# Performance work log

Measured on AMD Instinct MI355X. Metric: run time of the kernel, lower is better.

The kernel has to match this reference:

```python
import jax, jax.numpy as jnp
import numpy as np

DILATION = 6
KS = 3
N = KS * KS  # 9 kernel sample points
PAD = 1      # zero padding inside DeformConv2d
EPS = 1e-5


def conv2d(x, w, b=None, padding=0):
    out = jax.lax.conv_general_dilated(
        x, w, window_strides=(1, 1),
        padding=[(padding, padding), (padding, padding)],
        dimension_numbers=('NCHW', 'OIHW', 'NCHW'))
    if b is not None:
        out = out + b[None, :, None, None]
    return out


def batchnorm_train(x, gamma, beta):
    # training-mode BN (module default): batch statistics over (N,H,W)
    mean = x.mean(axis=(0, 2, 3), keepdims=True)
    var = x.var(axis=(0, 2, 3), keepdims=True)
    return gamma[None, :, None, None] * (x - mean) * jax.lax.rsqrt(var + EPS) + beta[None, :, None, None]


def deform_conv(x, p_w, p_b, m_w, m_b, d_w, d_b, w):
    b, c, h, wd = x.shape
    offset = conv2d(x, p_w, p_b, padding=1)                 # (b, 2N, h, w)
    m = jax.nn.sigmoid(conv2d(x, m_w, m_b, padding=1))      # (b, N, h, w) modulation
    s = 2.0 * jax.nn.sigmoid(conv2d(x, d_w, d_b, padding=1))  # (b,1,h,w) adaptive dilation scale (=1 at logit 0)
    xp = jnp.pad(x, ((0, 0), (0, 0), (PAD, PAD), (PAD, PAD)))
    Hp, Wp = h + 2 * PAD, wd + 2 * PAD
    # kernel grid p_n, row-major (kh, kw) to match conv weight layout
    rng = jnp.arange(-(KS - 1) // 2, (KS - 1) // 2 + 1, dtype=x.dtype)
    pn_x, pn_y = jnp.meshgrid(rng, rng, indexing='ij')
    pn_x, pn_y = pn_x.reshape(-1), pn_y.reshape(-1)          # (N,)
    # base sampling positions (offset by PAD into padded map)
    p0_x = jnp.arange(1, h + 1, dtype=x.dtype)[:, None, None]    # (h,1,1)
    p0_y = jnp.arange(1, wd + 1, dtype=x.dtype)[None, :, None]   # (1,w,1)
    off = offset.transpose(0, 2, 3, 1)   # (b,h,w,2N)
    s_ = s.transpose(0, 2, 3, 1)         # (b,h,w,1)
    px = p0_x + DILATION * s_ * pn_x + off[..., :N]   # (b,h,w,N)
    py = p0_y + DILATION * s_ * pn_y + off[..., N:]
    fx, fy = jnp.floor(px), jnp.floor(py)
    qx_lt = jnp.clip(fx, 0, Hp - 1).astype(jnp.int32)
    qy_lt = jnp.clip(fy, 0, Wp - 1).astype(jnp.int32)
    qx_rb = jnp.clip(fx + 1, 0, Hp - 1).astype(jnp.int32)
    qy_rb = jnp.clip(fy + 1, 0, Wp - 1).astype(jnp.int32)
    pxc = jnp.clip(px, 0, Hp - 1)
    pyc = jnp.clip(py, 0, Wp - 1)
    g_lt = (1 + (qx_lt - pxc)) * (1 + (qy_lt - pyc))
    g_rb = (1 - (qx_rb - pxc)) * (1 - (qy_rb - pyc))
    g_lb = (1 + (qx_lt - pxc)) * (1 - (qy_rb - pyc))
    g_rt = (1 - (qx_rb - pxc)) * (1 + (qy_lt - pyc))

    def gather(qx, qy):
        idx = (qx * Wp + qy).reshape(b, 1, -1)                    # (b,1,h*w*N)
        xf = xp.reshape(b, c, Hp * Wp)
        out = jnp.take_along_axis(xf, jnp.broadcast_to(idx, (b, c, idx.shape[-1])), axis=2)
        return out.reshape(b, c, h, wd, N)

    x_off = (g_lt[:, None] * gather(qx_lt, qy_lt)
             + g_rb[:, None] * gather(qx_rb, qy_rb)
             + g_lb[:, None] * gather(qx_lt, qy_rb)
             + g_rt[:, None] * gather(qx_rb, qy_lt))
    x_off = x_off * m.transpose(0, 2, 3, 1)[:, None]              # modulation
    # final 3x3 conv over gathered samples == contraction over (c, N)
    return jnp.einsum('bchwn,ocn->bohw', x_off, w.reshape(w.shape[0], c, N))


def setup_inputs() -> dict:
    key = jax.random.key(0)
    ks = jax.random.split(key, 12)
    cin, c1, c2 = 512, 256, 64
    b, h, w = 2, 96, 96
    def rn(k, shape, scale):
        return jax.random.normal(k, shape, dtype=jnp.float32) * scale
    return {
        'x': rn(ks[0], (b, cin, h, w), 1.0),
        'bn1_g': jnp.ones((cin,), jnp.float32),
        'bn1_b': jnp.zeros((cin,), jnp.float32),
        'conv1_w': rn(ks[1], (c1, cin, 1, 1), (1.0 / cin) ** 0.5),
        'conv1_b': jnp.zeros((c1,), jnp.float32),
        'bn2_g': jnp.ones((c1,), jnp.float32),
        'bn2_b': jnp.zeros((c1,), jnp.float32),
        'p_w': rn(ks[2], (2 * N, c1, 3, 3), 0.01),
        'p_b': jnp.zeros((2 * N,), jnp.float32),
        'm_w': rn(ks[3], (N, c1, 3, 3), 0.01),
        'm_b': jnp.zeros((N,), jnp.float32),
        'd_w': rn(ks[4], (1, c1, 3, 3), 0.01),
        'd_b': jnp.zeros((1,), jnp.float32),
        'dconv_w': rn(ks[5], (c2, c1, 3, 3), (1.0 / (c1 * 9)) ** 0.5),
    }


def reference(x, bn1_g, bn1_b, conv1_w, conv1_b, bn2_g, bn2_b,
              p_w, p_b, m_w, m_b, d_w, d_b, dconv_w):
    f = jax.nn.relu(batchnorm_train(x, bn1_g, bn1_b))
    f = conv2d(f, conv1_w, conv1_b)
    f = batchnorm_train(f, bn2_g, bn2_b)
    return deform_conv(f, p_w, p_b, m_w, m_b, d_w, d_b, dconv_w)
```

## Files before the change

kernel.cpp:

```cpp
#include <hip/hip_runtime.h>
#include <hip/hip_bf16.h>
#include <math.h>

#define BATCH 2
#define CIN 512
#define C1 256
#define C2 64
#define HH 96
#define WW 96
#define HWSZ 9216
#define NPIX 18432
#define HP 98
#define WP 98
#define PLSTRIDE 516096

typedef __attribute__((ext_vector_type(8))) short bf16x8;
typedef __attribute__((ext_vector_type(4))) short bf16x4;
typedef __attribute__((ext_vector_type(4))) float f32x4;
typedef __attribute__((ext_vector_type(4))) unsigned int u32x4;
typedef __attribute__((ext_vector_type(2))) unsigned int u32x2;
typedef unsigned short u16;
typedef unsigned int u32;

__device__ __forceinline__ float bfu2f(u16 u) {
  u32 v = ((u32)u) << 16; return __builtin_bit_cast(float, v);
}
__device__ __forceinline__ u16 f2bfu(float f) {
  return __builtin_bit_cast(u16, __float2bfloat16(f));
}
__device__ __forceinline__ float rd_any(const void* p, size_t i, int fl) {
  return fl ? bfu2f(((const u16*)p)[i]) : ((const float*)p)[i];
}
__device__ __forceinline__ int get_fl(const u32* g1raw) {
  return g1raw[0] != 0x3F800000u;
}
__device__ __forceinline__ bf16x8 lds_frag(const u16* p) {
  bf16x4 lo = *(const bf16x4*)p;
  bf16x4 hi = *(const bf16x4*)(p + 4);
  bf16x8 r;
  r[0] = lo[0]; r[1] = lo[1]; r[2] = lo[2]; r[3] = lo[3];
  r[4] = hi[0]; r[5] = hi[1]; r[6] = hi[2]; r[7] = hi[3];
  return r;
}
__device__ __forceinline__ void split4(const f32x4& v, u32x2& ph, u32x2& pl) {
  u16 h0 = f2bfu(v[0]), h1 = f2bfu(v[1]), h2 = f2bfu(v[2]), h3 = f2bfu(v[3]);
  u16 l0 = f2bfu(v[0] - bfu2f(h0)), l1 = f2bfu(v[1] - bfu2f(h1));
  u16 l2 = f2bfu(v[2] - bfu2f(h2)), l3 = f2bfu(v[3] - bfu2f(h3));
  ph = (u32x2){(u32)h0 | ((u32)h1 << 16), (u32)h2 | ((u32)h3 << 16)};
  pl = (u32x2){(u32)l0 | ((u32)l1 << 16), (u32)l2 | ((u32)l3 << 16)};
}

__global__ __launch_bounds__(256) void prep_kernel(
    const void* cw, const void* pw, const void* mw, const void* dw, const void* dcw,
    const void* cb, const void* g1, const void* b1, const void* g2, const void* b2,
    const void* pb, const void* mb, const void* db,
    u16* __restrict__ W1b, u16* __restrict__ W1l,
    u16* __restrict__ Wofa, u16* __restrict__ Wofal,
    u16* __restrict__ Wab, u16* __restrict__ Wabl,
    float* __restrict__ canon, float* __restrict__ statz, float* __restrict__ xpf) {
  int e = blockIdx.x * 256 + threadIdx.x;
  if (e >= 555036) return;
  int fl = get_fl((const u32*)g1);
  if (e < 131072) {
    float v = rd_any(cw, e, fl);
    u16 h = f2bfu(v);
    W1b[e] = h; W1l[e] = f2bfu(v - bfu2f(h));
  } else if (e < 204800) {
    int i = e - 131072;
    int tap = i >> 13; int r = i & 8191; int m = r >> 8; int c = r & 255;
    float v = 0.f;
    if (m < 18)       v = rd_any(pw, (size_t)(m * 256 + c) * 9 + tap, fl);
    else if (m < 27)  v = rd_any(mw, (size_t)((m - 18) * 256 + c) * 9 + tap, fl);
    else if (m == 27) v = rd_any(dw, (size_t)c * 9 + tap, fl);
    u16 h = f2bfu(v);
    Wofa[i] = h; Wofal[i] = f2bfu(v - bfu2f(h));
  } else if (e < 352256) {
    int i = e - 204800;
    int n = i >> 14; int r = i & 16383; int o = r >> 8; int c = r & 255;
    float v = rd_any(dcw, (size_t)(o * 256 + c) * 9 + n, fl);
    u16 h = f2bfu(v);
    Wab[i] = h; Wabl[i] = f2bfu(v - bfu2f(h));
  } else if (e < 354076) {
    int i = e - 352256;
    const void* src; int off;
    if      (i < 256)  { src = cb; off = i; }
    else if (i < 768)  { src = g1; off = i - 256; }
    else if (i < 1280) { src = b1; off = i - 768; }
    else if (i < 1536) { src = g2; off = i - 1280; }
    else if (i < 1792) { src = b2; off = i - 1536; }
    else if (i < 1810) { src = pb; off = i - 1792; }
    else if (i < 1819) { src = mb; off = i - 1810; }
    else               { src = db; off = i - 1819; }
    canon[i] = rd_any(src, off, fl);
  } else if (e < 356380) {
    statz[e - 354076] = 0.f;
  } else {
    int k = e - 356380;
    int ch = k & 255; int pxi = k >> 8;
    int bb = pxi / 388; int r = pxi % 388;
    int h, w;
    if (r < 98)      { h = 0;  w = r; }
    else if (r < 196){ h = 97; w = r - 98; }
    else if (r < 292){ h = r - 196 + 1; w = 0; }
    else             { h = r - 292 + 1; w = 97; }
    xpf[(((size_t)(bb * HP) + h) * WP + w) * C1 + ch] = 0.f;
  }
}

__global__ __launch_bounds__(256) void bn_stats_kernel(
    const void* __restrict__ x, const float* __restrict__ gamma,
    const float* __restrict__ beta, float* __restrict__ scale,
    float* __restrict__ shift, float* __restrict__ sums, float* __restrict__ sumsq,
    int* __restrict__ cnt, const u32* __restrict__ g1raw, int force, int C) {
  int c = blockIdx.x, part = blockIdx.y, tid = threadIdx.x;
  int fl = force ? 1 : get_fl(g1raw);
  int b = part >> 1, half = part & 1;
  size_t base = ((size_t)(b * C + c)) * HWSZ + half * (HWSZ / 2);
  float s = 0.f, q = 0.f;
  if (fl) {
    const u16* p = (const u16*)x + base;
    for (int i = tid; i < 576; i += 256) {
      u32x4 U = *(const u32x4*)(p + i * 8);
      #pragma unroll
      for (int k = 0; k < 4; ++k) {
        float v0 = bfu2f((u16)(U[k] & 0xffff));
        float v1 = bfu2f((u16)(U[k] >> 16));
        s += v0 + v1; q = fmaf(v0, v0, fmaf(v1, v1, q));
      }
    }
  } else {
    const float* p = (const float*)x + base;
    for (int i = tid; i < 1152; i += 256) {
      f32x4 v = *(const f32x4*)(p + i * 4);
      #pragma unroll
      for (int k = 0; k < 4; ++k) { s += v[k]; q = fmaf(v[k], v[k], q); }
    }
  }
  __shared__ float sh[512];
  sh[tid] = s; sh[tid + 256] = q;
  __syncthreads();
  for (int off = 128; off > 0; off >>= 1) {
    if (tid < off) { sh[tid] += sh[tid + off]; sh[tid + 256] += sh[tid + 256 + off]; }
    __syncthreads();
  }
  if (tid == 0) {
    atomicAdd(&sums[c], sh[0]);
    atomicAdd(&sumsq[c], sh[256]);
    __threadfence();
    int old = atomicAdd(&cnt[c], 1);
    if (old == 3) {
      float S = atomicAdd(&sums[c], 0.f);
      float Q = atomicAdd(&sumsq[c], 0.f);
      float mean = S * (1.f / (float)NPIX);
      float var  = fmaxf(Q * (1.f / (float)NPIX) - mean * mean, 0.f);
      float sc = gamma[c] * rsqrtf(var + 1e-5f);
      scale[c] = sc;
      shift[c] = beta[c] - mean * sc;
    }
  }
}

__global__ __launch_bounds__(256) void conv1x1_kernel(
    const void* __restrict__ x, const u16* __restrict__ W1b, const u16* __restrict__ W1l,
    const float* __restrict__ cb, const float* __restrict__ scale,
    const float* __restrict__ shift, const u32* __restrict__ g1raw,
    u16* __restrict__ f1) {
  __shared__ u16 Bh[2][64][68];
  __shared__ u16 Bl[2][64][68];
  int tid = threadIdx.x;
  int fl = get_fl(g1raw);
  int bxr = blockIdx.x;
  int bx = (bxr & 7) * 36 + (bxr >> 3);
  int p0 = bx * 64;
  int co0 = blockIdx.y * 128;
  int b = p0 / HWSZ;
  int hw0 = p0 % HWSZ;
  int lane = tid & 63, wv = tid >> 6, quad = lane >> 4, mr = lane & 15;
  int m0 = co0 + wv * 32;
  f32x4 acc[2][4];
  #pragma unroll
  for (int i = 0; i < 2; ++i)
    #pragma unroll
    for (int j = 0; j < 4; ++j) acc[i][j] = (f32x4){0.f, 0.f, 0.f, 0.f};

  int spx = tid & 63, cg = tid >> 6;
  int gpx = hw0 + spx;

  float pva[8], pvb[8];
  auto ISSUE = [&](int c0) {
    #pragma unroll
    for (int j = 0; j < 8; ++j) {
      int ci = c0 + cg * 16 + j * 2;
      if (fl) {
        const u16* xb = (const u16*)x;
        pva[j] = bfu2f(xb[((size_t)(b * CIN + ci)) * HWSZ + gpx]);
        pvb[j] = bfu2f(xb[((size_t)(b * CIN + ci + 1)) * HWSZ + gpx]);
      } else {
        const float* xf = (const float*)x;
        pva[j] = xf[((size_t)(b * CIN + ci)) * HWSZ + gpx];
        pvb[j] = xf[((size_t)(b * CIN + ci + 1)) * HWSZ + gpx];
      }
    }
  };
  auto COMBINE = [&](int buf, int c0) {
    #pragma unroll
    for (int j = 0; j < 8; ++j) {
      int ci = c0 + cg * 16 + j * 2;
      float v0 = fmaxf(fmaf(pva[j], scale[ci], shift[ci]), 0.f);
      float v1 = fmaxf(fmaf(pvb[j], scale[ci + 1], shift[ci + 1]), 0.f);
      u16 h0 = f2bfu(v0), h1 = f2bfu(v1);
      u16 l0 = f2bfu(v0 - bfu2f(h0)), l1 = f2bfu(v1 - bfu2f(h1));
      *(u32*)&Bh[buf][spx][cg * 16 + j * 2] = (u32)h0 | ((u32)h1 << 16);
      *(u32*)&Bl[buf][spx][cg * 16 + j * 2] = (u32)l0 | ((u32)l1 << 16);
    }
  };

  ISSUE(0);
  COMBINE(0, 0);
  for (int c8 = 0; c8 < 8; ++c8) {
    __syncthreads();
    if (c8 < 7) ISSUE((c8 + 1) * 64);
    int bsel = c8 & 1;
    int c0 = c8 * 64;
    #pragma unroll
    for (int kk2 = 0; kk2 < 2; ++kk2) {
      int kk = kk2 * 32;
      #pragma unroll
      for (int mf = 0; mf < 2; ++mf) {
        size_t wix = (size_t)(m0 + mf * 16 + mr) * CIN + c0 + kk + quad * 8;
        bf16x8 ah = *(const bf16x8*)(W1b + wix);
        bf16x8 al = *(const bf16x8*)(W1l + wix);
        #pragma unroll
        for (int nt = 0; nt < 4; ++nt) {
          bf16x8 bl = lds_frag(&Bl[bsel][nt * 16 + mr][kk + quad * 8]);
          bf16x8 bh = lds_frag(&Bh[bsel][nt * 16 + mr][kk + quad * 8]);
          acc[mf][nt] = __builtin_amdgcn_mfma_f32_16x16x32_bf16(ah, bl, acc[mf][nt], 0, 0, 0);
          acc[mf][nt] = __builtin_amdgcn_mfma_f32_16x16x32_bf16(al, bh, acc[mf][nt], 0, 0, 0);
          acc[mf][nt] = __builtin_amdgcn_mfma_f32_16x16x32_bf16(ah, bh, acc[mf][nt], 0, 0, 0);
        }
      }
    }
    if (c8 < 7) COMBINE(bsel ^ 1, (c8 + 1) * 64);
  }
  #pragma unroll
  for (int mf = 0; mf < 2; ++mf) {
    #pragma unroll
    for (int nt = 0; nt < 4; ++nt) {
      #pragma unroll
      for (int r = 0; r < 4; ++r) {
        int co = m0 + mf * 16 + quad * 4 + r;
        f1[((size_t)(b * C1 + co)) * HWSZ + hw0 + nt * 16 + mr] = f2bfu(acc[mf][nt][r] + cb[co]);
      }
    }
  }
}

__global__ __launch_bounds__(256) void bn2pad_kernel(
    const u16* __restrict__ f1, const float* __restrict__ scale,
    const float* __restrict__ shift, float* __restrict__ xpf) {
  int bid = blockIdx.x;
  int ht = bid % 144; int ct = (bid / 144) & 3; int b = bid / 576;
  int hw0 = ht * 64, c0 = ct * 64;
  __shared__ float t[64][65];
  int tid = threadIdx.x;
  #pragma unroll
  for (int it = 0; it < 16; ++it) {
    int e = it * 256 + tid;
    int p = e & 63, ci = e >> 6;
    float v = bfu2f(f1[((size_t)(b * C1 + c0 + ci)) * HWSZ + hw0 + p]);
    t[ci][p] = fmaf(v, scale[c0 + ci], shift[c0 + ci]);
  }
  __syncthreads();
  #pragma unroll
  for (int it = 0; it < 16; ++it) {
    int e = it * 256 + tid;
    int ci = e & 63, p = e >> 6;
    int hw = hw0 + p; int h = hw / WW; int w = hw % WW;
    xpf[(((size_t)(b * HP) + h + 1) * WP + w + 1) * C1 + c0 + ci] = t[ci][p];
  }
}

__global__ __launch_bounds__(256) void offconv_kernel(
    const float* __restrict__ xpf, const u16* __restrict__ Wofa, const u16* __restrict__ Wofal,
    const float* __restrict__ pbc, const float* __restrict__ mbc,
    const float* __restrict__ dbc, float* __restrict__ opart3) {
  __shared__ u16 Vh[2][32][68];
  __shared__ u16 Vl[2][32][68];
  int tid = threadIdx.x;
  int bxr = blockIdx.x;
  int bx = (bxr & 7) * 72 + (bxr >> 3);
  int tg = blockIdx.y;
  int p0 = bx * 32;
  int b = p0 / HWSZ;
  int hw = p0 % HWSZ; int h0 = hw / WW; int w0 = hw % WW;
  int lane = tid & 63, wv = tid >> 6, quad = lane >> 4, mr = lane & 15;
  int m0 = (wv & 1) * 16;
  int ntile = wv >> 1;
  int srow = tid >> 4;
  int scol = (tid & 15) * 4;
  f32x4 acc = (f32x4){0.f, 0.f, 0.f, 0.f};

  f32x4 pvA[2], pvB[2];
  auto ISSUE = [&](f32x4 (&pv)[2], int it) {
    int tap = tg * 3 + (it >> 2);
    int th = tap / 3, tw = tap % 3;
    int c0 = (it & 3) * 64;
    const float* base = xpf + ((size_t)(b * HP + h0 + th) * WP + (w0 + tw)) * C1;
    #pragma unroll
    for (int pass = 0; pass < 2; ++pass) {
      int px = pass * 16 + srow;
      pv[pass] = *(const f32x4*)(base + (size_t)px * C1 + c0 + scol);
    }
  };
  auto COMBINE = [&](f32x4 (&pv)[2], int buf) {
    #pragma unroll
    for (int pass = 0; pass < 2; ++pass) {
      int px = pass * 16 + srow;
      u32x2 ph, pl;
      split4(pv[pass], ph, pl);
      *(u32x2*)&Vh[buf][px][scol] = ph;
      *(u32x2*)&Vl[buf][px][scol] = pl;
    }
  };
  auto MFMA_STEP = [&](int bsel, int it) {
    int tap = tg * 3 + (it >> 2);
    int c0 = (it & 3) * 64;
    #pragma unroll
    for (int kk2 = 0; kk2 < 2; ++kk2) {
      int kof = kk2 * 32 + quad * 8;
      size_t wix = (size_t)(tap * 32 + m0 + mr) * C1 + c0 + kof;
      bf16x8 ah = *(const bf16x8*)(Wofa + wix);
      bf16x8 al = *(const bf16x8*)(Wofal + wix);
      bf16x8 bl = lds_frag(&Vl[bsel][ntile * 16 + mr][kof]);
      bf16x8 bh = lds_frag(&Vh[bsel][ntile * 16 + mr][kof]);
      acc = __builtin_amdgcn_mfma_f32_16x16x32_bf16(ah, bl, acc, 0, 0, 0);
      acc = __builtin_amdgcn_mfma_f32_16x16x32_bf16(al, bh, acc, 0, 0, 0);
      acc = __builtin_amdgcn_mfma_f32_16x16x32_bf16(ah, bh, acc, 0, 0, 0);
    }
  };

  ISSUE(pvA, 0);
  ISSUE(pvB, 1);
  COMBINE(pvA, 0);
  for (int it = 0; it < 12; it += 2) {
    __syncthreads();
    if (it + 2 < 12) ISSUE(pvA, it + 2);
    MFMA_STEP(0, it);
    COMBINE(pvB, 1);
    __syncthreads();
    if (it + 3 < 12) ISSUE(pvB, it + 3);
    MFMA_STEP(1, it + 1);
    if (it + 2 < 12) COMBINE(pvA, 0);
  }
  float* plane = opart3 + (size_t)tg * PLSTRIDE;
  int px = ntile * 16 + mr;
  #pragma unroll
  for (int r = 0; r < 4; ++r) {
    int m = m0 + quad * 4 + r;
    if (m < 28) {
      float v = acc[r];
      if (tg == 0) v += (m < 18) ? pbc[m] : ((m < 27) ? mbc[m - 18] : dbc[0]);
      plane[(size_t)m * NPIX + p0 + px] = v;
    }
  }
}

__global__ __launch_bounds__(256) void deform_kernel(
    const float* __restrict__ xpf, const u16* __restrict__ Wab, const u16* __restrict__ Wabl,
    const float* __restrict__ opart3, float* __restrict__ planes3) {
  __shared__ u16   Vh[2][32][68];
  __shared__ u16   Vl[2][32][68];
  __shared__ int   smi[3][4][32];
  __shared__ float smw[3][4][32];
  int tid = threadIdx.x;
  int bxr = blockIdx.x;
  int bx = (bxr & 7) * 72 + (bxr >> 3);
  int g = blockIdx.y;
  int p0 = bx * 32;
  int b = p0 / HWSZ;
  int hw0 = p0 % HWSZ;

  if (tid < 96) {
    int nn = tid >> 5;
    int p = tid & 31;
    int n = g * 3 + nn;
    int bp = p0 + p;
    int hw = hw0 + p; int h = hw / WW; int w = hw % WW;
    const float* P0 = opart3;
    const float* P1 = opart3 + PLSTRIDE;
    const float* P2 = opart3 + 2 * PLSTRIDE;
    size_t iox = (size_t)n * NPIX + bp;
    size_t ioy = (size_t)(9 + n) * NPIX + bp;
    size_t iml = (size_t)(18 + n) * NPIX + bp;
    size_t isl = (size_t)27 * NPIX + bp;
    float offx = P0[iox] + P1[iox] + P2[iox];
    float offy = P0[ioy] + P1[ioy] + P2[ioy];
    float mlog = P0[iml] + P1[iml] + P2[iml];
    float slog = P0[isl] + P1[isl] + P2[isl];
    float mm = 1.f / (1.f + expf(-mlog));
    float s  = 2.f / (1.f + expf(-slog));
    float pnx = (float)(n / 3 - 1), pny = (float)(n % 3 - 1);
    float px = (float)(h + 1) + 6.f * s * pnx + offx;
    float py = (float)(w + 1) + 6.f * s * pny + offy;
    float fx = floorf(px), fy = floorf(py);
    float qxlt = fminf(fmaxf(fx, 0.f), 97.f);
    float qylt = fminf(fmaxf(fy, 0.f), 97.f);
    float qxrb = fminf(fmaxf(fx + 1.f, 0.f), 97.f);
    float qyrb = fminf(fmaxf(fy + 1.f, 0.f), 97.f);
    float pxc = fminf(fmaxf(px, 0.f), 97.f);
    float pyc = fminf(fmaxf(py, 0.f), 97.f);
    float glt = (1.f + (qxlt - pxc)) * (1.f + (qylt - pyc));
    float grb = (1.f - (qxrb - pxc)) * (1.f - (qyrb - pyc));
    float glb = (1.f + (qxlt - pxc)) * (1.f - (qyrb - pyc));
    float grt = (1.f - (qxrb - pxc)) * (1.f + (qylt - pyc));
    int ixlt = (int)qxlt, iylt = (int)qylt, ixrb = (int)qxrb, iyrb = (int)qyrb;
    int base = b * (HP * WP);
    smi[nn][0][p] = base + ixlt * WP + iylt;  smw[nn][0][p] = glt * mm;
    smi[nn][1][p] = base + ixrb * WP + iyrb;  smw[nn][1][p] = grb * mm;
    smi[nn][2][p] = base + ixlt * WP + iyrb;  smw[nn][2][p] = glb * mm;
    smi[nn][3][p] = base + ixrb * WP + iylt;  smw[nn][3][p] = grt * mm;
  }
  __syncthreads();

  int lane = tid & 63, wv = tid >> 6, quad = lane >> 4, mr = lane & 15;
  int m0 = wv * 16;
  int srow = tid >> 4;
  int scol = (tid & 15) * 4;
  f32x4 acc[2];
  acc[0] = (f32x4){0.f, 0.f, 0.f, 0.f};
  acc[1] = (f32x4){0.f, 0.f, 0.f, 0.f};

  f32x4 pvA[2][4], pvB[2][4];
  auto ISSUE = [&](f32x4 (&pv)[2][4], int it) {
    int nn = it >> 2; int c0 = (it & 3) * 64;
    #pragma unroll
    for (int pass = 0; pass < 2; ++pass) {
      int px = pass * 16 + srow;
      #pragma unroll
      for (int k = 0; k < 4; ++k)
        pv[pass][k] = *(const f32x4*)(xpf + (size_t)smi[nn][k][px] * C1 + c0 + scol);
    }
  };
  auto COMBINE = [&](f32x4 (&pv)[2][4], int buf, int it) {
    int nn = it >> 2;
    #pragma unroll
    for (int pass = 0; pass < 2; ++pass) {
      int px = pass * 16 + srow;
      float w0 = smw[nn][0][px], w1 = smw[nn][1][px], w2 = smw[nn][2][px], w3 = smw[nn][3][px];
      f32x4 vc;
      #pragma unroll
      for (int j = 0; j < 4; ++j)
        vc[j] = fmaf(w0, pv[pass][0][j],
                fmaf(w1, pv[pass][1][j],
                fmaf(w2, pv[pass][2][j], w3 * pv[pass][3][j])));
      u32x2 ph, pl;
      split4(vc, ph, pl);
      *(u32x2*)&Vh[buf][px][scol] = ph;
      *(u32x2*)&Vl[buf][px][scol] = pl;
    }
  };
  auto MFMA_STEP = [&](int bsel, int it) {
    int n = g * 3 + (it >> 2); int c0 = (it & 3) * 64;
    #pragma unroll
    for (int kk2 = 0; kk2 < 2; ++kk2) {
      int kof = kk2 * 32 + quad * 8;
      size_t wix = (size_t)(n * C2 + m0 + mr) * C1 + c0 + kof;
      bf16x8 ah = *(const bf16x8*)(Wab + wix);
      bf16x8 al = *(const bf16x8*)(Wabl + wix);
      #pragma unroll
      for (int nt = 0; nt < 2; ++nt) {
        bf16x8 bl = lds_frag(&Vl[bsel][nt * 16 + mr][kof]);
        bf16x8 bh = lds_frag(&Vh[bsel][nt * 16 + mr][kof]);
        acc[nt] = __builtin_amdgcn_mfma_f32_16x16x32_bf16(ah, bl, acc[nt], 0, 0, 0);
        acc[nt] = __builtin_amdgcn_mfma_f32_16x16x32_bf16(al, bh, acc[nt], 0, 0, 0);
        acc[nt] = __builtin_amdgcn_mfma_f32_16x16x32_bf16(ah, bh, acc[nt], 0, 0, 0);
      }
    }
  };

  ISSUE(pvA, 0);
  ISSUE(pvB, 1);
  COMBINE(pvA, 0, 0);
  for (int it = 0; it < 12; it += 2) {
    __syncthreads();
    if (it + 2 < 12) ISSUE(pvA, it + 2);
    MFMA_STEP(0, it);
    COMBINE(pvB, 1, it + 1);
    __syncthreads();
    if (it + 3 < 12) ISSUE(pvB, it + 3);
    MFMA_STEP(1, it + 1);
    if (it + 2 < 12) COMBINE(pvA, 0, it + 2);
  }
  #pragma unroll
  for (int nt = 0; nt < 2; ++nt) {
    #pragma unroll
    for (int r = 0; r < 4; ++r) {
      int o = m0 + quad * 4 + r;
      planes3[((size_t)g * C2 + o) * NPIX + p0 + nt * 16 + mr] = acc[nt][r];
    }
  }
}

__global__ __launch_bounds__(256) void reduce_kernel(
    const float* __restrict__ planes3, const u32* __restrict__ g1raw,
    void* __restrict__ outv) {
  int t = blockIdx.x * 256 + threadIdx.x;
  int e4 = t * 4;
  int b = e4 / (C2 * HWSZ);
  int rem = e4 % (C2 * HWSZ);
  int o = rem / HWSZ;
  int hw = rem % HWSZ;
  size_t src = (size_t)o * NPIX + b * HWSZ + hw;
  f32x4 v0 = *(const f32x4*)(planes3 + src);
  f32x4 v1 = *(const f32x4*)(planes3 + (size_t)C2 * NPIX + src);
  f32x4 v2 = *(const f32x4*)(planes3 + 2 * (size_t)C2 * NPIX + src);
  f32x4 sum;
  #pragma unroll
  for (int j = 0; j < 4; ++j) sum[j] = v0[j] + v1[j] + v2[j];
  if (get_fl(g1raw)) {
    u16* ob = (u16*)outv;
    #pragma unroll
    for (int j = 0; j < 4; ++j) ob[e4 + j] = f2bfu(sum[j]);
  } else {
    *(f32x4*)((float*)outv + e4) = sum;
  }
}

extern "C" void kernel_launch(void* const* d_in, const int* in_sizes, int n_in,
                              void* d_out, int out_size, void* d_ws, size_t ws_size,
                              hipStream_t stream) {
  const void* x       = d_in[0];
  const void* bn1_g   = d_in[1];
  const void* bn1_b   = d_in[2];
  const void* conv1_w = d_in[3];
  const void* conv1_b = d_in[4];
  const void* bn2_g   = d_in[5];
  const void* bn2_b   = d_in[6];
  const void* p_w     = d_in[7];
  const void* p_b     = d_in[8];
  const void* m_w     = d_in[9];
  const void* m_b     = d_in[10];
  const void* d_w     = d_in[11];
  const void* d_b     = d_in[12];
  const void* dconv_w = d_in[13];
  const u32* g1raw = (const u32*)bn1_g;

  float* ws = (float*)d_ws;
  float* canon = ws + 16;
  float* cbc = canon + 0;
  float* g1c = canon + 256;
  float* b1c = canon + 768;
  float* g2c = canon + 1280;
  float* b2c = canon + 1536;
  float* pbc = canon + 1792;
  float* mbc = canon + 1810;
  float* dbc = canon + 1819;
  float* scale1 = ws + 1840;
  float* shift1 = ws + 2352;
  float* scale2 = ws + 2864;
  float* shift2 = ws + 3120;
  float* statz  = ws + 3376;
  float* sums1  = statz;
  float* sumsq1 = statz + 512;
  int*   cnt1   = (int*)(statz + 1024);
  float* sums2  = statz + 1536;
  float* sumsq2 = statz + 1792;
  int*   cnt2   = (int*)(statz + 2048);
  u16* W1b   = (u16*)(ws + 5680);
  u16* W1l   = (u16*)(ws + 71216);
  u16* Wofa  = (u16*)(ws + 136752);
  u16* Wofal = (u16*)(ws + 173616);
  u16* Wab   = (u16*)(ws + 210480);
  u16* Wabl  = (u16*)(ws + 284208);
  u16* f1    = (u16*)(ws + 357936);
  float* opart3 = ws + 357936;
  float* xpf    = ws + 2717232;
  float* planes3 = ws + 7634480;

  prep_kernel<<<2169, 256, 0, stream>>>(conv1_w, p_w, m_w, d_w, dconv_w,
                                        conv1_b, bn1_g, bn1_b, bn2_g, bn2_b,
                                        p_b, m_b, d_b,
                                        W1b, W1l, Wofa, Wofal, Wab, Wabl, canon, statz, xpf);
  bn_stats_kernel<<<dim3(CIN, 4), 256, 0, stream>>>(x, g1c, b1c, scale1, shift1,
                                                    sums1, sumsq1, cnt1, g1raw, 0, CIN);
  conv1x1_kernel<<<dim3(288, 2), 256, 0, stream>>>(x, W1b, W1l, cbc, scale1, shift1, g1raw, f1);
  bn_stats_kernel<<<dim3(C1, 4), 256, 0, stream>>>(f1, g2c, b2c, scale2, shift2,
                                                   sums2, sumsq2, cnt2, g1raw, 1, C1);
  bn2pad_kernel<<<1152, 256, 0, stream>>>(f1, scale2, shift2, xpf);
  offconv_kernel<<<dim3(576, 3), 256, 0, stream>>>(xpf, Wofa, Wofal, pbc, mbc, dbc, opart3);
  deform_kernel<<<dim3(576, 3), 256, 0, stream>>>(xpf, Wab, Wabl, opart3, planes3);
  reduce_kernel<<<1152, 256, 0, stream>>>(planes3, g1raw, d_out);
}
```

Before: 311.9 us.

## Retile conv1x1 to 16-pixel blocks covering all channels; single-buffer deform gather

The conv1x1 kernel now gives each block 16 pixels and all 256 output channels, where before it took 64 pixels and 128 channels. That makes 1152 blocks instead of 576, and the x input is read once per pixel rather than twice across the two channel halves. The kernel prefetches with two register buffers and shares each B fragment across four M tiles. The deform kernel goes back to a single register prefetch buffer, which lowers register pressure but leaves fewer gathers in flight. The trade-off is more reloading of the weight matrix per pixel, and the narrow 16-pixel tiles may give weaker coalescing on the x loads and f1 stores.

```diff
diff --git a/kernel.cpp b/kernel.cpp
--- a/kernel.cpp
+++ b/kernel.cpp
@@ -165,92 +165,82 @@
     const float* __restrict__ cb, const float* __restrict__ scale,
     const float* __restrict__ shift, const u32* __restrict__ g1raw,
     u16* __restrict__ f1) {
-  __shared__ u16 Bh[2][64][68];
-  __shared__ u16 Bl[2][64][68];
+  __shared__ u16 Bh[2][16][68];
+  __shared__ u16 Bl[2][16][68];
   int tid = threadIdx.x;
   int fl = get_fl(g1raw);
   int bxr = blockIdx.x;
-  int bx = (bxr & 7) * 36 + (bxr >> 3);
-  int p0 = bx * 64;
-  int co0 = blockIdx.y * 128;
+  int bx = (bxr & 7) * 144 + (bxr >> 3);
+  int p0 = bx * 16;
   int b = p0 / HWSZ;
   int hw0 = p0 % HWSZ;
   int lane = tid & 63, wv = tid >> 6, quad = lane >> 4, mr = lane & 15;
-  int m0 = co0 + wv * 32;
-  f32x4 acc[2][4];
-  #pragma unroll
-  for (int i = 0; i < 2; ++i)
-    #pragma unroll
-    for (int j = 0; j < 4; ++j) acc[i][j] = (f32x4){0.f, 0.f, 0.f, 0.f};
-
-  int spx = tid & 63, cg = tid >> 6;
+  int m0 = wv * 64;
+  f32x4 acc[4];
+  #pragma unroll
+  for (int j = 0; j < 4; ++j) acc[j] = (f32x4){0.f, 0.f, 0.f, 0.f};
+
+  int spx = tid & 15, cg = tid >> 4;
   int gpx = hw0 + spx;
 
-  float pva[8], pvb[8];
-  auto ISSUE = [&](int c0) {
-    #pragma unroll
-    for (int j = 0; j < 8; ++j) {
-      int ci = c0 + cg * 16 + j * 2;
-      if (fl) {
-        const u16* xb = (const u16*)x;
-        pva[j] = bfu2f(xb[((size_t)(b * CIN + ci)) * HWSZ + gpx]);
-        pvb[j] = bfu2f(xb[((size_t)(b * CIN + ci + 1)) * HWSZ + gpx]);
-      } else {
-        const float* xf = (const float*)x;
-        pva[j] = xf[((size_t)(b * CIN + ci)) * HWSZ + gpx];
-        pvb[j] = xf[((size_t)(b * CIN + ci + 1)) * HWSZ + gpx];
-      }
-    }
-  };
-  auto COMBINE = [&](int buf, int c0) {
-    #pragma unroll
-    for (int j = 0; j < 8; ++j) {
-      int ci = c0 + cg * 16 + j * 2;
-      float v0 = fmaxf(fmaf(pva[j], scale[ci], shift[ci]), 0.f);
-      float v1 = fmaxf(fmaf(pvb[j], scale[ci + 1], shift[ci + 1]), 0.f);
+  float pvA[4], pvB[4];
+  auto ISSUE = [&](float (&pv)[4], int c0) {
+    #pragma unroll
+    for (int j = 0; j < 4; ++j) {
+      int ci = c0 + cg * 4 + j;
+      pv[j] = fl ? bfu2f(((const u16*)x)[((size_t)(b * CIN + ci)) * HWSZ + gpx])
+                 : ((const float*)x)[((size_t)(b * CIN + ci)) * HWSZ + gpx];
+    }
+  };
+  auto COMBINE = [&](float (&pv)[4], int buf, int c0) {
+    #pragma unroll
+    for (int k = 0; k < 2; ++k) {
+      int ci = c0 + cg * 4 + k * 2;
+      float v0 = fmaxf(fmaf(pv[k * 2], scale[ci], shift[ci]), 0.f);
+      float v1 = fmaxf(fmaf(pv[k * 2 + 1], scale[ci + 1], shift[ci + 1]), 0.f);
       u16 h0 = f2bfu(v0), h1 = f2bfu(v1);
       u16 l0 = f2bfu(v0 - bfu2f(h0)), l1 = f2bfu(v1 - bfu2f(h1));
-      *(u32*)&Bh[buf][spx][cg * 16 + j * 2] = (u32)h0 | ((u32)h1 << 16);
-      *(u32*)&Bl[buf][spx][cg * 16 + j * 2] = (u32)l0 | ((u32)l1 << 16);
-    }
-  };
-
-  ISSUE(0);
-  COMBINE(0, 0);
-  for (int c8 = 0; c8 < 8; ++c8) {
-    __syncthreads();
-    if (c8 < 7) ISSUE((c8 + 1) * 64);
-    int bsel = c8 & 1;
-    int c0 = c8 * 64;
+      *(u32*)&Bh[buf][spx][cg * 4 + k * 2] = (u32)h0 | ((u32)h1 << 16);
+      *(u32*)&Bl[buf][spx][cg * 4 + k * 2] = (u32)l0 | ((u32)l1 << 16);
+    }
+  };
+  auto MFMA_STEP = [&](int bsel, int c0) {
     #pragma unroll
     for (int kk2 = 0; kk2 < 2; ++kk2) {
       int kk = kk2 * 32;
+      bf16x8 bl = lds_frag(&Bl[bsel][mr][kk + quad * 8]);
+      bf16x8 bh = lds_frag(&Bh[bsel][mr][kk + quad * 8]);
       #pragma unroll
-      for (int mf = 0; mf < 2; ++mf) {
+      for (int mf = 0; mf < 4; ++mf) {
         size_t wix = (size_t)(m0 + mf * 16 + mr) * CIN + c0 + kk + quad * 8;
         bf16x8 ah = *(const bf16x8*)(W1b + wix);
         bf16x8 al = *(const bf16x8*)(W1l + wix);
-        #pragma unroll
-        for (int nt = 0; nt < 4; ++nt) {
-          bf16x8 bl = lds_frag(&Bl[bsel][nt * 16 + mr][kk + quad * 8]);
-          bf16x8 bh = lds_frag(&Bh[bsel][nt * 16 + mr][kk + quad * 8]);
-          acc[mf][nt] = __builtin_amdgcn_mfma_f32_16x16x32_bf16(ah, bl, acc[mf][nt], 0, 0, 0);
-          acc[mf][nt] = __builtin_amdgcn_mfma_f32_16x16x32_bf16(al, bh, acc[mf][nt], 0, 0, 0);
-          acc[mf][nt] = __builtin_amdgcn_mfma_f32_16x16x32_bf16(ah, bh, acc[mf][nt], 0, 0, 0);
-        }
+        acc[mf] = __builtin_amdgcn_mfma_f32_16x16x32_bf16(ah, bl, acc[mf], 0, 0, 0);
+        acc[mf] = __builtin_amdgcn_mfma_f32_16x16x32_bf16(al, bh, acc[mf], 0, 0, 0);
+        acc[mf] = __builtin_amdgcn_mfma_f32_16x16x32_bf16(ah, bh, acc[mf], 0, 0, 0);
       }
     }
-    if (c8 < 7) COMBINE(bsel ^ 1, (c8 + 1) * 64);
-  }
-  #pragma unroll
-  for (int mf = 0; mf < 2; ++mf) {
-    #pragma unroll
-    for (int nt = 0; nt < 4; ++nt) {
-      #pragma unroll
-      for (int r = 0; r < 4; ++r) {
-        int co = m0 + mf * 16 + quad * 4 + r;
-        f1[((size_t)(b * C1 + co)) * HWSZ + hw0 + nt * 16 + mr] = f2bfu(acc[mf][nt][r] + cb[co]);
-      }
+  };
+
+  ISSUE(pvA, 0);
+  ISSUE(pvB, 64);
+  COMBINE(pvA, 0, 0);
+  for (int c8 = 0; c8 < 8; c8 += 2) {
+    __syncthreads();
+    if (c8 + 2 < 8) ISSUE(pvA, (c8 + 2) * 64);
+    MFMA_STEP(0, c8 * 64);
+    COMBINE(pvB, 1, (c8 + 1) * 64);
+    __syncthreads();
+    if (c8 + 3 < 8) ISSUE(pvB, (c8 + 3) * 64);
+    MFMA_STEP(1, (c8 + 1) * 64);
+    if (c8 + 2 < 8) COMBINE(pvA, 0, (c8 + 2) * 64);
+  }
+  #pragma unroll
+  for (int mf = 0; mf < 4; ++mf) {
+    #pragma unroll
+    for (int r = 0; r < 4; ++r) {
+      int co = m0 + mf * 16 + quad * 4 + r;
+      f1[((size_t)(b * C1 + co)) * HWSZ + hw0 + mr] = f2bfu(acc[mf][r] + cb[co]);
     }
   }
 }
@@ -430,8 +420,8 @@
   acc[0] = (f32x4){0.f, 0.f, 0.f, 0.f};
   acc[1] = (f32x4){0.f, 0.f, 0.f, 0.f};
 
-  f32x4 pvA[2][4], pvB[2][4];
-  auto ISSUE = [&](f32x4 (&pv)[2][4], int it) {
+  f32x4 pv[2][4];
+  auto ISSUE = [&](int it) {
     int nn = it >> 2; int c0 = (it & 3) * 64;
     #pragma unroll
     for (int pass = 0; pass < 2; ++pass) {
@@ -441,7 +431,7 @@
         pv[pass][k] = *(const f32x4*)(xpf + (size_t)smi[nn][k][px] * C1 + c0 + scol);
     }
   };
-  auto COMBINE = [&](f32x4 (&pv)[2][4], int buf, int it) {
+  auto COMBINE = [&](int buf, int it) {
     int nn = it >> 2;
     #pragma unroll
     for (int pass = 0; pass < 2; ++pass) {
@@ -459,7 +449,13 @@
       *(u32x2*)&Vl[buf][px][scol] = pl;
     }
   };
-  auto MFMA_STEP = [&](int bsel, int it) {
+
+  ISSUE(0);
+  COMBINE(0, 0);
+  for (int it = 0; it < 12; ++it) {
+    __syncthreads();
+    if (it < 11) ISSUE(it + 1);
+    int bsel = it & 1;
     int n = g * 3 + (it >> 2); int c0 = (it & 3) * 64;
     #pragma unroll
     for (int kk2 = 0; kk2 < 2; ++kk2) {
@@ -476,20 +472,7 @@
         acc[nt] = __builtin_amdgcn_mfma_f32_16x16x32_bf16(ah, bh, acc[nt], 0, 0, 0);
       }
     }
-  };
-
-  ISSUE(pvA, 0);
-  ISSUE(pvB, 1);
-  COMBINE(pvA, 0, 0);
-  for (int it = 0; it < 12; it += 2) {
-    __syncthreads();
-    if (it + 2 < 12) ISSUE(pvA, it + 2);
-    MFMA_STEP(0, it);
-    COMBINE(pvB, 1, it + 1);
-    __syncthreads();
-    if (it + 3 < 12) ISSUE(pvB, it + 3);
-    MFMA_STEP(1, it + 1);
-    if (it + 2 < 12) COMBINE(pvA, 0, it + 2);
+    if (it < 11) COMBINE(bsel ^ 1, it + 1);
   }
   #pragma unroll
   for (int nt = 0; nt < 2; ++nt) {
@@ -583,7 +566,7 @@
                                         W1b, W1l, Wofa, Wofal, Wab, Wabl, canon, statz, xpf);
   bn_stats_kernel<<<dim3(CIN, 4), 256, 0, stream>>>(x, g1c, b1c, scale1, shift1,
                                                     sums1, sumsq1, cnt1, g1raw, 0, CIN);
-  conv1x1_kernel<<<dim3(288, 2), 256, 0, stream>>>(x, W1b, W1l, cbc, scale1, shift1, g1raw, f1);
+  conv1x1_kernel<<<1152, 256, 0, stream>>>(x, W1b, W1l, cbc, scale1, shift1, g1raw, f1);
   bn_stats_kernel<<<dim3(C1, 4), 256, 0, stream>>>(f1, g2c, b2c, scale2, shift2,
                                                    sums2, sumsq2, cnt2, g1raw, 1, C1);
   bn2pad_kernel<<<1152, 256, 0, stream>>>(f1, scale2, shift2, xpf);
```

After: 374.5 us. 20.1% more time.

## Fuse BN2 statistics into conv1x1 epilogue and single-buffer deform gather prefetch

Applied to the files above, without the earlier changes.

Accumulates per-channel sum and sum-of-squares of the rounded conv1x1 outputs inside the conv1x1 epilogue. Partials are reduced with lane shuffles and atomics, and the last-arriving block computes the BN2 scale and shift, so the separate bn_stats pass over f1 and its launch go away. The deform kernel's gather prefetch is also cut from two register buffers to one, reducing register pressure at the cost of a shallower load-ahead. The atomic count threshold assumes exactly 288 contributing blocks per channel.

```diff
diff --git a/kernel.cpp b/kernel.cpp
--- a/kernel.cpp
+++ b/kernel.cpp
@@ -164,7 +164,10 @@
     const void* __restrict__ x, const u16* __restrict__ W1b, const u16* __restrict__ W1l,
     const float* __restrict__ cb, const float* __restrict__ scale,
     const float* __restrict__ shift, const u32* __restrict__ g1raw,
-    u16* __restrict__ f1) {
+    u16* __restrict__ f1,
+    const float* __restrict__ g2c, const float* __restrict__ b2c,
+    float* __restrict__ sums2, float* __restrict__ sumsq2, int* __restrict__ cnt2,
+    float* __restrict__ scale2, float* __restrict__ shift2) {
   __shared__ u16 Bh[2][64][68];
   __shared__ u16 Bl[2][64][68];
   int tid = threadIdx.x;
@@ -242,6 +245,11 @@
     }
     if (c8 < 7) COMBINE(bsel ^ 1, (c8 + 1) * 64);
   }
+  float sp[2][4], qp[2][4];
+  #pragma unroll
+  for (int mf = 0; mf < 2; ++mf)
+    #pragma unroll
+    for (int r = 0; r < 4; ++r) { sp[mf][r] = 0.f; qp[mf][r] = 0.f; }
   #pragma unroll
   for (int mf = 0; mf < 2; ++mf) {
     #pragma unroll
@@ -249,7 +257,38 @@
       #pragma unroll
       for (int r = 0; r < 4; ++r) {
         int co = m0 + mf * 16 + quad * 4 + r;
-        f1[((size_t)(b * C1 + co)) * HWSZ + hw0 + nt * 16 + mr] = f2bfu(acc[mf][nt][r] + cb[co]);
+        u16 hv = f2bfu(acc[mf][nt][r] + cb[co]);
+        f1[((size_t)(b * C1 + co)) * HWSZ + hw0 + nt * 16 + mr] = hv;
+        float vr = bfu2f(hv);
+        sp[mf][r] += vr; qp[mf][r] = fmaf(vr, vr, qp[mf][r]);
+      }
+    }
+  }
+  #pragma unroll
+  for (int mf = 0; mf < 2; ++mf) {
+    #pragma unroll
+    for (int r = 0; r < 4; ++r) {
+      float s = sp[mf][r], q = qp[mf][r];
+      #pragma unroll
+      for (int m = 1; m < 16; m <<= 1) {
+        s += __shfl_xor(s, m);
+        q += __shfl_xor(q, m);
+      }
+      if (mr == 0) {
+        int co = m0 + mf * 16 + quad * 4 + r;
+        atomicAdd(&sums2[co], s);
+        atomicAdd(&sumsq2[co], q);
+        __threadfence();
+        int old = atomicAdd(&cnt2[co], 1);
+        if (old == 287) {
+          float S = atomicAdd(&sums2[co], 0.f);
+          float Q = atomicAdd(&sumsq2[co], 0.f);
+          float mean = S * (1.f / (float)NPIX);
+          float var  = fmaxf(Q * (1.f / (float)NPIX) - mean * mean, 0.f);
+          float sc = g2c[co] * rsqrtf(var + 1e-5f);
+          scale2[co] = sc;
+          shift2[co] = b2c[co] - mean * sc;
+        }
       }
     }
   }
@@ -430,8 +469,8 @@
   acc[0] = (f32x4){0.f, 0.f, 0.f, 0.f};
   acc[1] = (f32x4){0.f, 0.f, 0.f, 0.f};
 
-  f32x4 pvA[2][4], pvB[2][4];
-  auto ISSUE = [&](f32x4 (&pv)[2][4], int it) {
+  f32x4 pv[2][4];
+  auto ISSUE = [&](int it) {
     int nn = it >> 2; int c0 = (it & 3) * 64;
     #pragma unroll
     for (int pass = 0; pass < 2; ++pass) {
@@ -441,7 +480,7 @@
         pv[pass][k] = *(const f32x4*)(xpf + (size_t)smi[nn][k][px] * C1 + c0 + scol);
     }
   };
-  auto COMBINE = [&](f32x4 (&pv)[2][4], int buf, int it) {
+  auto COMBINE = [&](int buf, int it) {
     int nn = it >> 2;
     #pragma unroll
     for (int pass = 0; pass < 2; ++pass) {
@@ -459,7 +498,13 @@
       *(u32x2*)&Vl[buf][px][scol] = pl;
     }
   };
-  auto MFMA_STEP = [&](int bsel, int it) {
+
+  ISSUE(0);
+  COMBINE(0, 0);
+  for (int it = 0; it < 12; ++it) {
+    __syncthreads();
+    if (it < 11) ISSUE(it + 1);
+    int bsel = it & 1;
     int n = g * 3 + (it >> 2); int c0 = (it & 3) * 64;
     #pragma unroll
     for (int kk2 = 0; kk2 < 2; ++kk2) {
@@ -476,20 +521,7 @@
         acc[nt] = __builtin_amdgcn_mfma_f32_16x16x32_bf16(ah, bh, acc[nt], 0, 0, 0);
       }
     }
-  };
-
-  ISSUE(pvA, 0);
-  ISSUE(pvB, 1);
-  COMBINE(pvA, 0, 0);
-  for (int it = 0; it < 12; it += 2) {
-    __syncthreads();
-    if (it + 2 < 12) ISSUE(pvA, it + 2);
-    MFMA_STEP(0, it);
-    COMBINE(pvB, 1, it + 1);
-    __syncthreads();
-    if (it + 3 < 12) ISSUE(pvB, it + 3);
-    MFMA_STEP(1, it + 1);
-    if (it + 2 < 12) COMBINE(pvA, 0, it + 2);
+    if (it < 11) COMBINE(bsel ^ 1, it + 1);
   }
   #pragma unroll
   for (int nt = 0; nt < 2; ++nt) {
@@ -583,9 +615,8 @@
                                         W1b, W1l, Wofa, Wofal, Wab, Wabl, canon, statz, xpf);
   bn_stats_kernel<<<dim3(CIN, 4), 256, 0, stream>>>(x, g1c, b1c, scale1, shift1,
                                                     sums1, sumsq1, cnt1, g1raw, 0, CIN);
-  conv1x1_kernel<<<dim3(288, 2), 256, 0, stream>>>(x, W1b, W1l, cbc, scale1, shift1, g1raw, f1);
-  bn_stats_kernel<<<dim3(C1, 4), 256, 0, stream>>>(f1, g2c, b2c, scale2, shift2,
-                                                   sums2, sumsq2, cnt2, g1raw, 1, C1);
+  conv1x1_kernel<<<dim3(288, 2), 256, 0, stream>>>(x, W1b, W1l, cbc, scale1, shift1, g1raw, f1,
+                                                   g2c, b2c, sums2, sumsq2, cnt2, scale2, shift2);
   bn2pad_kernel<<<1152, 256, 0, stream>>>(f1, scale2, shift2, xpf);
   offconv_kernel<<<dim3(576, 3), 256, 0, stream>>>(xpf, Wofa, Wofal, pbc, mbc, dbc, opart3);
   deform_kernel<<<dim3(576, 3), 256, 0, stream>>>(xpf, Wab, Wabl, opart3, planes3);
```

Result: slower. 613.9 us (+96.8%).
